# Performance work log

Hardware: AMD Instinct MI355X
Metric: run time of the kernel (lower is better)

## Reference

```python
import jax, jax.numpy as jnp
import numpy as np

N = 100000
E = 1600000
F_NODE = 6
F_EDGE = 2
H = 64


def _glorot(key, shape):
    lim = float(np.sqrt(6.0 / (shape[0] + shape[1])))
    return jax.random.uniform(key, shape, jnp.float32, -lim, lim)


def setup_inputs() -> dict:
    key = jax.random.key(0)
    ks = jax.random.split(key, 16)
    inp = {
        "x": jax.random.normal(ks[0], (N, F_NODE), jnp.float32),
        "edge_index": jax.random.randint(ks[1], (2, E), 0, N, jnp.int64),
        "edge_attr": jax.random.normal(ks[2], (E, F_EDGE), jnp.float32),
        # GCN layers (PyG GCNConv: linear no-bias, then aggregate, then +bias)
        "W1": _glorot(ks[3], (F_NODE, H)), "b1": jnp.zeros((H,), jnp.float32),
        "W2": _glorot(ks[4], (H, H)), "b2": jnp.zeros((H,), jnp.float32),
        "W3": _glorot(ks[5], (H, H)), "b3": jnp.zeros((H,), jnp.float32),
        # edge_mlp
        "We1": _glorot(ks[6], (F_EDGE, H)), "be1": jnp.zeros((H,), jnp.float32),
        "We2": _glorot(ks[7], (H, H)), "be2": jnp.zeros((H,), jnp.float32),
        # predictor
        "Wp1": _glorot(ks[8], (3 * H, H)), "bp1": jnp.zeros((H,), jnp.float32),
        "Wp2": _glorot(ks[9], (H, H // 2)), "bp2": jnp.zeros((H // 2,), jnp.float32),
        "Wp3": _glorot(ks[10], (H // 2, 1)), "bp3": jnp.zeros((1,), jnp.float32),
    }
    return inp


def _gcn_conv(h, W, b, src_sl, dst_sl, norm, n):
    # PyG GCNConv with self-loops and symmetric normalization
    h = h @ W                                   # [N, H_out]
    msg = h[src_sl] * norm[:, None]             # gather + scale per edge(+loop)
    out = jax.ops.segment_sum(msg, dst_sl, num_segments=n)
    return out + b


def _forward(x, edge_attr, W1, b1, W2, b2, W3, b3, We1, be1, We2, be2,
             Wp1, bp1, Wp2, bp2, Wp3, bp3, edge_index):
    n = x.shape[0]
    src, dst = edge_index[0], edge_index[1]

    # --- edge feature injection (vectorized version of per-edge loop) ---
    ef = jax.nn.relu(edge_attr @ We1 + be1) @ We2 + be2      # [E, H]
    nef = (jax.ops.segment_sum(ef, src, num_segments=n)
           + jax.ops.segment_sum(ef, dst, num_segments=n))   # [N, H]
    ones_e = jnp.ones((ef.shape[0],), x.dtype)
    deg = (jax.ops.segment_sum(ones_e, src, num_segments=n)
           + jax.ops.segment_sum(ones_e, dst, num_segments=n))
    deg = jnp.maximum(deg, 1.0)
    nef = nef / deg[:, None]
    # hidden_dim (64) >= node feature dim (6) -> truncate
    x = x + nef[:, : x.shape[1]] * 0.5

    # --- GCN normalization with self-loops (shared across layers) ---
    loop = jnp.arange(n, dtype=src.dtype)
    src_sl = jnp.concatenate([src, loop])
    dst_sl = jnp.concatenate([dst, loop])
    deg_sl = jax.ops.segment_sum(jnp.ones_like(dst_sl, dtype=x.dtype), dst_sl,
                                 num_segments=n)
    dinv = jnp.where(deg_sl > 0, deg_sl ** -0.5, 0.0)
    norm = dinv[src_sl] * dinv[dst_sl]

    h = jax.nn.relu(_gcn_conv(x, W1, b1, src_sl, dst_sl, norm, n))
    h = jax.nn.relu(_gcn_conv(h, W2, b2, src_sl, dst_sl, norm, n))
    h = _gcn_conv(h, W3, b3, src_sl, dst_sl, norm, n)

    graph_emb = h.mean(axis=0)                 # global_mean_pool, batch=None
    node_mean = h.mean(axis=0)
    node_std = jnp.std(h, axis=0, ddof=1)      # torch.std is unbiased
    combined = jnp.concatenate([graph_emb, node_mean, node_std])  # [3H]

    p = jax.nn.relu(combined @ Wp1 + bp1)      # dropout inactive in eval
    p = jax.nn.relu(p @ Wp2 + bp2)
    out = jax.nn.sigmoid(p @ Wp3 + bp3)        # (1,)
    return out


def reference(x, edge_index, edge_attr, W1, b1, W2, b2, W3, b3,
              We1, be1, We2, be2, Wp1, bp1, Wp2, bp2, Wp3, bp3):
    return _forward(x, edge_attr, W1, b1, W2, b2, W3, b3, We1, be1, We2, be2,
                    Wp1, bp1, Wp2, bp2, Wp3, bp3, edge_index)
```

## Files before the change

### kernel.cpp

```cpp
#include <hip/hip_runtime.h>
#include <hip/hip_bf16.h>
#include <stdint.h>

typedef float floatx2 __attribute__((ext_vector_type(2)));

#define NPB 256
#define NB 391
#define NBLKA 512

__device__ __forceinline__ float rdlane(float v, int l) {
    return __uint_as_float(__builtin_amdgcn_readlane(__float_as_uint(v), l));
}
__device__ __forceinline__ unsigned pk_fp8x4(float a, float b, float c, float d) {
    int u = __builtin_amdgcn_cvt_pk_fp8_f32(a, b, 0, false);
    u = __builtin_amdgcn_cvt_pk_fp8_f32(c, d, u, true);
    return (unsigned)u;
}
__device__ __forceinline__ unsigned pk_fp8x2(float a, float b) {
    return (unsigned)__builtin_amdgcn_cvt_pk_fp8_f32(a, b, 0, false);
}

__global__ __launch_bounds__(512) void k_zero(int* __restrict__ inTot,
                                              double* __restrict__ sums) {
    int t = threadIdx.x;
    if (t < 128) sums[t] = 0.0;
    if (t < NB) inTot[t] = 0;
}

__global__ __launch_bounds__(256) void k_A1(const int* __restrict__ ei,
                                            int* __restrict__ h,
                                            int* __restrict__ inTot,
                                            int E, int epb) {
    __shared__ int hist[NB], histIn[NB];
    int t = threadIdx.x, blk = blockIdx.x;
    for (int b = t; b < NB; b += 256) { hist[b] = 0; histIn[b] = 0; }
    __syncthreads();
    int e0 = blk * epb, e1 = min(E, e0 + epb);
    for (int e = e0 + t; e < e1; e += 256) {
        int s = ei[e], d = ei[E + e];
        atomicAdd(&hist[s >> 8], 1);
        atomicAdd(&hist[d >> 8], 1);
        atomicAdd(&histIn[d >> 8], 1);
    }
    __syncthreads();
    for (int b = t; b < NB; b += 256) {
        h[(size_t)b * NBLKA + blk] = hist[b];
        if (histIn[b]) atomicAdd(&inTot[b], histIn[b]);
    }
}

__global__ __launch_bounds__(512) void k_sc1(const int* __restrict__ v,
                                             int* __restrict__ bsum, int n) {
    __shared__ int l[512];
    int i = blockIdx.x * 512 + threadIdx.x;
    l[threadIdx.x] = (i < n) ? v[i] : 0;
    __syncthreads();
    for (int s = 256; s > 0; s >>= 1) {
        if (threadIdx.x < s) l[threadIdx.x] += l[threadIdx.x + s];
        __syncthreads();
    }
    if (threadIdx.x == 0) bsum[blockIdx.x] = l[0];
}
__global__ __launch_bounds__(512) void k_sc2(int* __restrict__ bsum, int nb) {
    __shared__ int l[512];
    int t = threadIdx.x;
    int v = (t < nb) ? bsum[t] : 0;
    l[t] = v;
    __syncthreads();
    for (int s = 1; s < 512; s <<= 1) {
        int tmp = (t >= s) ? l[t - s] : 0;
        __syncthreads();
        l[t] += tmp;
        __syncthreads();
    }
    if (t < nb) bsum[t] = l[t] - v;
}
__global__ __launch_bounds__(512) void k_sc3(int* __restrict__ v,
                                             const int* __restrict__ bsum, int n) {
    __shared__ int l[512];
    int i = blockIdx.x * 512 + threadIdx.x;
    int x = (i < n) ? v[i] : 0;
    l[threadIdx.x] = x;
    __syncthreads();
    for (int s = 1; s < 512; s <<= 1) {
        int tmp = (threadIdx.x >= (unsigned)s) ? l[threadIdx.x - s] : 0;
        __syncthreads();
        l[threadIdx.x] += tmp;
        __syncthreads();
    }
    if (i < n) v[i] = l[threadIdx.x] - x + bsum[blockIdx.x];
}
__global__ __launch_bounds__(512) void k_scanIn(const int* __restrict__ inTot,
                                                int* __restrict__ inBase) {
    __shared__ int l[512];
    int t = threadIdx.x;
    int v = (t < NB) ? inTot[t] : 0;
    l[t] = v;
    __syncthreads();
    for (int s = 1; s < 512; s <<= 1) {
        int tmp = (t >= s) ? l[t - s] : 0;
        __syncthreads();
        l[t] += tmp;
        __syncthreads();
    }
    if (t < NB) inBase[t] = l[t] - v;
}

__global__ __launch_bounds__(256) void k_A2(
    const int* __restrict__ ei, const float* __restrict__ ea,
    const float* __restrict__ We1, const float* __restrict__ be1,
    const float* __restrict__ We2, const float* __restrict__ be2,
    const int* __restrict__ hs, uint4* __restrict__ rec, int E, int epb) {
    __shared__ float sWe1[128], sbe1[64], sWe2[64 * 6], sbe2[6];
    __shared__ int cur[NB];
    int t = threadIdx.x, blk = blockIdx.x;
    if (t < 128) sWe1[t] = We1[t];
    if (t < 64) {
        sbe1[t] = be1[t];
#pragma unroll
        for (int c = 0; c < 6; ++c) sWe2[t * 6 + c] = We2[t * 64 + c];
    }
    if (t < 6) sbe2[t] = be2[t];
    for (int b = t; b < NB; b += 256) cur[b] = hs[(size_t)b * NBLKA + blk];
    __syncthreads();

    int e0 = blk * epb, e1 = min(E, e0 + epb);
    for (int e = e0 + t; e < e1; e += 256) {
        int s = ei[e], d = ei[E + e];
        float2 aa = ((const float2*)ea)[e];
        float acc[6];
#pragma unroll
        for (int c = 0; c < 6; ++c) acc[c] = sbe2[c];
#pragma unroll
        for (int j = 0; j < 64; ++j) {
            float hh = fmaf(aa.x, sWe1[j], fmaf(aa.y, sWe1[64 + j], sbe1[j]));
            hh = fmaxf(hh, 0.f);
#pragma unroll
            for (int c = 0; c < 6; ++c) acc[c] = fmaf(hh, sWe2[j * 6 + c], acc[c]);
        }
        unsigned z = pk_fp8x4(acc[0], acc[1], acc[2], acc[3]);
        unsigned w = pk_fp8x2(acc[4], acc[5]);
        int p0 = atomicAdd(&cur[s >> 8], 1);
        rec[p0] = make_uint4((unsigned)(s << 1), 0u, z, w);
        int p1 = atomicAdd(&cur[d >> 8], 1);
        rec[p1] = make_uint4((unsigned)(d << 1) | 1u, (unsigned)s, z, w);
    }
}

__global__ __launch_bounds__(256) void k_B(
    const uint4* __restrict__ rec, const int* __restrict__ hs,
    const int* __restrict__ inBase, const float* __restrict__ x,
    float* __restrict__ xp, float* __restrict__ dinv,
    int* __restrict__ offI, int* __restrict__ in_src, int E, int N) {
    __shared__ float nef[NPB * 6];
    __shared__ int degAll[NPB], degIn[NPB], rnk[NPB], sc[NPB], exO[NPB];
    int t = threadIdx.x, b = blockIdx.x;
#pragma unroll
    for (int c = 0; c < 6; ++c) nef[t * 6 + c] = 0.f;
    degAll[t] = 0; degIn[t] = 0; rnk[t] = 0;
    __syncthreads();

    int rb = hs[(size_t)b * NBLKA];
    int re = (b == NB - 1) ? 2 * E : hs[(size_t)(b + 1) * NBLKA];
    for (int j = rb + t; j < re; j += 256) {
        uint4 r = rec[j];
        int l = (int)((r.x >> 1) & 255u);
        atomicAdd(&degAll[l], 1);
        if (r.x & 1u) atomicAdd(&degIn[l], 1);
        floatx2 p01 = __builtin_amdgcn_cvt_pk_f32_fp8(r.z, false);
        floatx2 p23 = __builtin_amdgcn_cvt_pk_f32_fp8(r.z, true);
        floatx2 p45 = __builtin_amdgcn_cvt_pk_f32_fp8(r.w, false);
        atomicAdd(&nef[l * 6 + 0], p01.x);
        atomicAdd(&nef[l * 6 + 1], p01.y);
        atomicAdd(&nef[l * 6 + 2], p23.x);
        atomicAdd(&nef[l * 6 + 3], p23.y);
        atomicAdd(&nef[l * 6 + 4], p45.x);
        atomicAdd(&nef[l * 6 + 5], p45.y);
    }
    __syncthreads();

    int v = degIn[t];
    sc[t] = v;
    __syncthreads();
    for (int s = 1; s < 256; s <<= 1) {
        int tmp = (t >= s) ? sc[t - s] : 0;
        __syncthreads();
        sc[t] += tmp;
        __syncthreads();
    }
    exO[t] = sc[t] - v;
    __syncthreads();

    int node = b * NPB + t;
    int ib = inBase[b];
    if (node <= N) offI[node] = ib + exO[t];
    if (node < N) {
        float da = (float)degAll[t];
        float inv = 0.5f / fmaxf(da, 1.f);
        const float2* xr = (const float2*)(x + (size_t)node * 6);
        float2 x01 = xr[0], x23 = xr[1], x45 = xr[2];
        float2* xw = (float2*)(xp + (size_t)node * 6);
        xw[0] = make_float2(x01.x + nef[t * 6 + 0] * inv, x01.y + nef[t * 6 + 1] * inv);
        xw[1] = make_float2(x23.x + nef[t * 6 + 2] * inv, x23.y + nef[t * 6 + 3] * inv);
        xw[2] = make_float2(x45.x + nef[t * 6 + 4] * inv, x45.y + nef[t * 6 + 5] * inv);
        dinv[node] = 1.f / sqrtf(1.f + (float)degIn[t]);
    }
    __syncthreads();

    for (int j = rb + t; j < re; j += 256) {
        uint4 r = rec[j];
        if (r.x & 1u) {
            int l = (int)((r.x >> 1) & 255u);
            int k = atomicAdd(&rnk[l], 1);
            in_src[ib + exO[l] + k] = (int)r.y;
        }
    }
}

__global__ __launch_bounds__(256) void k_mm1(const float* __restrict__ xp,
                                             const float* __restrict__ W1,
                                             const float* __restrict__ dinv,
                                             unsigned* __restrict__ sOut, int n) {
    int lane = threadIdx.x & 63;
    int sub = lane & 15;
    int wid = (blockIdx.x * blockDim.x + threadIdx.x) >> 6;
    int nw = (gridDim.x * blockDim.x) >> 6;
    float w[6];
#pragma unroll
    for (int c = 0; c < 6; ++c) w[c] = W1[c * 64 + lane];
    for (int i = wid; i < n; i += nw) {
        float xv = (lane < 6) ? xp[(size_t)i * 6 + lane] : 0.f;
        float acc = 0.f;
#pragma unroll
        for (int c = 0; c < 6; ++c) acc = fmaf(rdlane(xv, c), w[c], acc);
        float o = acc * dinv[i];
        float o0 = __shfl(o, sub * 4 + 0);
        float o1 = __shfl(o, sub * 4 + 1);
        float o2 = __shfl(o, sub * 4 + 2);
        float o3 = __shfl(o, sub * 4 + 3);
        if (lane < 16) sOut[(size_t)i * 16 + lane] = pk_fp8x4(o0, o1, o2, o3);
    }
}

__global__ __launch_bounds__(256) void k_gathermm(
    const int* __restrict__ offI, const int* __restrict__ in_src,
    const float* __restrict__ dinv, const unsigned* __restrict__ sIn,
    const float* __restrict__ bias, const float* __restrict__ W,
    unsigned* __restrict__ sOut, int n) {
    int lane = threadIdx.x & 63;
    int sub = lane & 15, grp = lane >> 4;
    int wid = (blockIdx.x * blockDim.x + threadIdx.x) >> 6;
    int nw = (gridDim.x * blockDim.x) >> 6;
    float w[64];
#pragma unroll
    for (int c = 0; c < 64; ++c) w[c] = W[c * 64 + lane];
    float4 bb = ((const float4*)bias)[sub];

    for (int i = wid; i < n; i += nw) {
        unsigned su = sIn[(size_t)i * 16 + sub];
        float a0, a1, a2, a3;
        if (grp == 0) {
            floatx2 lo = __builtin_amdgcn_cvt_pk_f32_fp8(su, false);
            floatx2 hi = __builtin_amdgcn_cvt_pk_f32_fp8(su, true);
            a0 = lo.x; a1 = lo.y; a2 = hi.x; a3 = hi.y;
        } else { a0 = a1 = a2 = a3 = 0.f; }
        int b0 = offI[i], e0 = offI[i + 1];
#pragma unroll 4
        for (int j = b0 + grp; j < e0; j += 4) {
            unsigned src = (unsigned)in_src[j];
            unsigned u = sIn[(size_t)src * 16 + sub];
            floatx2 lo = __builtin_amdgcn_cvt_pk_f32_fp8(u, false);
            floatx2 hi = __builtin_amdgcn_cvt_pk_f32_fp8(u, true);
            a0 += lo.x; a1 += lo.y; a2 += hi.x; a3 += hi.y;
        }
        a0 += __shfl_xor(a0, 16); a1 += __shfl_xor(a1, 16);
        a2 += __shfl_xor(a2, 16); a3 += __shfl_xor(a3, 16);
        a0 += __shfl_xor(a0, 32); a1 += __shfl_xor(a1, 32);
        a2 += __shfl_xor(a2, 32); a3 += __shfl_xor(a3, 32);

        float dv = dinv[i];
        float h0 = fmaxf(fmaf(a0, dv, bb.x), 0.f);
        float h1 = fmaxf(fmaf(a1, dv, bb.y), 0.f);
        float h2 = fmaxf(fmaf(a2, dv, bb.z), 0.f);
        float h3 = fmaxf(fmaf(a3, dv, bb.w), 0.f);
        float o = 0.f;
#pragma unroll
        for (int g = 0; g < 16; ++g) {
            o = fmaf(rdlane(h0, g), w[g * 4 + 0], o);
            o = fmaf(rdlane(h1, g), w[g * 4 + 1], o);
            o = fmaf(rdlane(h2, g), w[g * 4 + 2], o);
            o = fmaf(rdlane(h3, g), w[g * 4 + 3], o);
        }
        o *= dv;
        float o0 = __shfl(o, sub * 4 + 0);
        float o1 = __shfl(o, sub * 4 + 1);
        float o2 = __shfl(o, sub * 4 + 2);
        float o3 = __shfl(o, sub * 4 + 3);
        if (lane < 16) sOut[(size_t)i * 16 + lane] = pk_fp8x4(o0, o1, o2, o3);
    }
}

__global__ __launch_bounds__(256) void k_gatherreduce(
    const int* __restrict__ offI, const int* __restrict__ in_src,
    const float* __restrict__ dinv, const unsigned* __restrict__ sIn,
    const float* __restrict__ b3, double* __restrict__ sums, int n) {
    int lane = threadIdx.x & 63;
    int sub = lane & 15, grp = lane >> 4;
    int wv = threadIdx.x >> 6;
    int wid = (blockIdx.x * blockDim.x + threadIdx.x) >> 6;
    int nw = (gridDim.x * blockDim.x) >> 6;
    float4 bb = ((const float4*)b3)[sub];
    double s0 = 0.0, s1 = 0.0, s2_ = 0.0, s3 = 0.0;
    double q0 = 0.0, q1 = 0.0, q2 = 0.0, q3 = 0.0;

    for (int i = wid; i < n; i += nw) {
        unsigned su = sIn[(size_t)i * 16 + sub];
        float a0, a1, a2, a3;
        if (grp == 0) {
            floatx2 lo = __builtin_amdgcn_cvt_pk_f32_fp8(su, false);
            floatx2 hi = __builtin_amdgcn_cvt_pk_f32_fp8(su, true);
            a0 = lo.x; a1 = lo.y; a2 = hi.x; a3 = hi.y;
        } else { a0 = a1 = a2 = a3 = 0.f; }
        int b0 = offI[i], e0 = offI[i + 1];
#pragma unroll 4
        for (int j = b0 + grp; j < e0; j += 4) {
            unsigned src = (unsigned)in_src[j];
            unsigned u = sIn[(size_t)src * 16 + sub];
            floatx2 lo = __builtin_amdgcn_cvt_pk_f32_fp8(u, false);
            floatx2 hi = __builtin_amdgcn_cvt_pk_f32_fp8(u, true);
            a0 += lo.x; a1 += lo.y; a2 += hi.x; a3 += hi.y;
        }
        a0 += __shfl_xor(a0, 16); a1 += __shfl_xor(a1, 16);
        a2 += __shfl_xor(a2, 16); a3 += __shfl_xor(a3, 16);
        a0 += __shfl_xor(a0, 32); a1 += __shfl_xor(a1, 32);
        a2 += __shfl_xor(a2, 32); a3 += __shfl_xor(a3, 32);

        float dv = dinv[i];
        float v0 = fmaf(a0, dv, bb.x);
        float v1 = fmaf(a1, dv, bb.y);
        float v2 = fmaf(a2, dv, bb.z);
        float v3 = fmaf(a3, dv, bb.w);
        s0 += v0; s1 += v1; s2_ += v2; s3 += v3;
        q0 += (double)v0 * v0; q1 += (double)v1 * v1;
        q2 += (double)v2 * v2; q3 += (double)v3 * v3;
    }
    __shared__ double shS[4 * 64], shQ[4 * 64];
    if (grp == 0) {
#pragma unroll
        for (int k = 0; k < 4; ++k) {
            double sk = (k == 0) ? s0 : (k == 1) ? s1 : (k == 2) ? s2_ : s3;
            double qk = (k == 0) ? q0 : (k == 1) ? q1 : (k == 2) ? q2 : q3;
            shS[wv * 64 + sub * 4 + k] = sk;
            shQ[wv * 64 + sub * 4 + k] = qk;
        }
    }
    __syncthreads();
    if (wv == 0) {
        double a = shS[lane] + shS[64 + lane] + shS[128 + lane] + shS[192 + lane];
        double c = shQ[lane] + shQ[64 + lane] + shQ[128 + lane] + shQ[192 + lane];
        unsafeAtomicAdd(&sums[lane], a);
        unsafeAtomicAdd(&sums[64 + lane], c);
    }
}

__global__ void k_head(const double* __restrict__ sums,
                       const float* __restrict__ Wp1, const float* __restrict__ bp1,
                       const float* __restrict__ Wp2, const float* __restrict__ bp2,
                       const float* __restrict__ Wp3, const float* __restrict__ bp3,
                       float* __restrict__ out, int n) {
    __shared__ float comb[192], p1[64], p2[32];
    int t = threadIdx.x;
    if (t < 64) {
        double s = sums[t], s2 = sums[64 + t];
        double m = s / n;
        double var = (s2 - s * s / n) / (double)(n - 1);
        float mf = (float)m;
        float sd = (float)sqrt(var > 0.0 ? var : 0.0);
        comb[t] = mf;
        comb[64 + t] = mf;
        comb[128 + t] = sd;
    }
    __syncthreads();
    if (t < 64) {
        float acc = bp1[t];
        for (int k = 0; k < 192; ++k) acc = fmaf(comb[k], Wp1[k * 64 + t], acc);
        p1[t] = fmaxf(acc, 0.f);
    }
    __syncthreads();
    if (t < 32) {
        float acc = bp2[t];
        for (int k = 0; k < 64; ++k) acc = fmaf(p1[k], Wp2[k * 32 + t], acc);
        p2[t] = fmaxf(acc, 0.f);
    }
    __syncthreads();
    if (t == 0) {
        float acc = bp3[0];
        for (int k = 0; k < 32; ++k) acc = fmaf(p2[k], Wp3[k], acc);
        out[0] = 1.f / (1.f + expf(-acc));
    }
}

static inline char* align16(char* p) {
    return (char*)(((uintptr_t)p + 15) & ~(uintptr_t)15);
}

extern "C" void kernel_launch(void* const* d_in, const int* in_sizes, int n_in,
                              void* d_out, int out_size, void* d_ws, size_t ws_size,
                              hipStream_t stream) {
    const float* x   = (const float*)d_in[0];
    const int*   ei  = (const int*)d_in[1];
    const float* ea  = (const float*)d_in[2];
    const float* W1  = (const float*)d_in[3];
    const float* b1  = (const float*)d_in[4];
    const float* W2  = (const float*)d_in[5];
    const float* b2  = (const float*)d_in[6];
    const float* W3  = (const float*)d_in[7];
    const float* b3  = (const float*)d_in[8];
    const float* We1 = (const float*)d_in[9];
    const float* be1 = (const float*)d_in[10];
    const float* We2 = (const float*)d_in[11];
    const float* be2 = (const float*)d_in[12];
    const float* Wp1 = (const float*)d_in[13];
    const float* bp1 = (const float*)d_in[14];
    const float* Wp2 = (const float*)d_in[15];
    const float* bp2 = (const float*)d_in[16];
    const float* Wp3 = (const float*)d_in[17];
    const float* bp3 = (const float*)d_in[18];

    const int N = in_sizes[0] / 6;
    const int E = in_sizes[1] / 2;
    const int epb = (E + NBLKA - 1) / NBLKA;
    const int HSZ = NB * NBLKA;
    const int nScan = (HSZ + 511) / 512;
    const size_t SB = (size_t)N * 64;

    char* p = (char*)d_ws;
    double* sums = (double*)p;          p = align16(p + 128 * sizeof(double));
    int* inTot = (int*)p;               p = align16(p + NB * 4);
    int* inBase = (int*)p;              p = align16(p + NB * 4);
    int* bsum = (int*)p;                p = align16(p + 512 * 4);
    int* h = (int*)p;                   p = align16(p + (size_t)HSZ * 4);
    float* xp = (float*)p;              p = align16(p + (size_t)N * 6 * 4);
    float* dinv = (float*)p;            p = align16(p + (size_t)N * 4);
    int* offI = (int*)p;                p = align16(p + ((size_t)N + 1) * 4);
    int* in_src = (int*)p;              p = align16(p + (size_t)E * 4);
    char* u = p;
    uint4* rec = (uint4*)u;
    unsigned* sbufA = (unsigned*)u;
    unsigned* sbufB = (unsigned*)(u + ((SB + 15) & ~(size_t)15));

    dim3 blk(256);

    k_zero<<<dim3(1), dim3(512), 0, stream>>>(inTot, sums);
    k_A1<<<dim3(NBLKA), blk, 0, stream>>>(ei, h, inTot, E, epb);
    k_sc1<<<dim3(nScan), dim3(512), 0, stream>>>(h, bsum, HSZ);
    k_sc2<<<dim3(1), dim3(512), 0, stream>>>(bsum, nScan);
    k_sc3<<<dim3(nScan), dim3(512), 0, stream>>>(h, bsum, HSZ);
    k_scanIn<<<dim3(1), dim3(512), 0, stream>>>(inTot, inBase);
    k_A2<<<dim3(NBLKA), blk, 0, stream>>>(ei, ea, We1, be1, We2, be2, h, rec, E, epb);
    k_B<<<dim3(NB), blk, 0, stream>>>(rec, h, inBase, x, xp, dinv, offI, in_src, E, N);

    k_mm1<<<dim3(1024), blk, 0, stream>>>(xp, W1, dinv, sbufA, N);
    k_gathermm<<<dim3(2048), blk, 0, stream>>>(offI, in_src, dinv, sbufA, b1, W2, sbufB, N);
    k_gathermm<<<dim3(2048), blk, 0, stream>>>(offI, in_src, dinv, sbufB, b2, W3, sbufA, N);
    k_gatherreduce<<<dim3(2048), blk, 0, stream>>>(offI, in_src, dinv, sbufA, b3, sums, N);
    k_head<<<dim3(1), dim3(64), 0, stream>>>(sums, Wp1, bp1, Wp2, bp2, Wp3, bp3,
                                             (float*)d_out, N);
}
```

Before: 615.5 us.

## Move edge MLP into histogram pass and widen node buckets to 512

The per-edge MLP and fp8 packing move from the scatter kernel k_A2 into the histogram kernel k_A1, which writes packed edge features to a new buffer that k_A2 then reads. The aim is to shorten the atomic-heavy scatter pass and give the histogram pass arithmetic to hide its memory latency. Node buckets grow from 256 to 512 nodes, so there are fewer buckets (196), fewer partition blocks (128), k_B runs with 512 threads, and the histogram scan is smaller. The cost is an extra E*8-byte buffer written and read back, and only 128 blocks in the A passes, which may not fill the GPU.

Result: slower. 752.9 us (+22.3%).

```diff
diff --git a/kernel.cpp b/kernel.cpp
--- a/kernel.cpp
+++ b/kernel.cpp
@@ -4,9 +4,9 @@
 
 typedef float floatx2 __attribute__((ext_vector_type(2)));
 
-#define NPB 256
-#define NB 391
-#define NBLKA 512
+#define NPB 512
+#define NB 196
+#define NBLKA 128
 
 __device__ __forceinline__ float rdlane(float v, int l) {
     return __uint_as_float(__builtin_amdgcn_readlane(__float_as_uint(v), l));
@@ -27,20 +27,44 @@
     if (t < NB) inTot[t] = 0;
 }
 
-__global__ __launch_bounds__(256) void k_A1(const int* __restrict__ ei,
-                                            int* __restrict__ h,
-                                            int* __restrict__ inTot,
-                                            int E, int epb) {
+__global__ __launch_bounds__(256) void k_A1(
+    const int* __restrict__ ei, const float* __restrict__ ea,
+    const float* __restrict__ We1, const float* __restrict__ be1,
+    const float* __restrict__ We2, const float* __restrict__ be2,
+    uint2* __restrict__ efp, int* __restrict__ h, int* __restrict__ inTot,
+    int E, int epb) {
+    __shared__ float sWe1[128], sbe1[64], sWe2[64 * 6], sbe2[6];
     __shared__ int hist[NB], histIn[NB];
     int t = threadIdx.x, blk = blockIdx.x;
+    if (t < 128) sWe1[t] = We1[t];
+    if (t < 64) {
+        sbe1[t] = be1[t];
+#pragma unroll
+        for (int c = 0; c < 6; ++c) sWe2[t * 6 + c] = We2[t * 64 + c];
+    }
+    if (t < 6) sbe2[t] = be2[t];
     for (int b = t; b < NB; b += 256) { hist[b] = 0; histIn[b] = 0; }
     __syncthreads();
+
     int e0 = blk * epb, e1 = min(E, e0 + epb);
     for (int e = e0 + t; e < e1; e += 256) {
         int s = ei[e], d = ei[E + e];
-        atomicAdd(&hist[s >> 8], 1);
-        atomicAdd(&hist[d >> 8], 1);
-        atomicAdd(&histIn[d >> 8], 1);
+        atomicAdd(&hist[s >> 9], 1);
+        atomicAdd(&hist[d >> 9], 1);
+        atomicAdd(&histIn[d >> 9], 1);
+        float2 aa = ((const float2*)ea)[e];
+        float acc[6];
+#pragma unroll
+        for (int c = 0; c < 6; ++c) acc[c] = sbe2[c];
+#pragma unroll
+        for (int j = 0; j < 64; ++j) {
+            float hh = fmaf(aa.x, sWe1[j], fmaf(aa.y, sWe1[64 + j], sbe1[j]));
+            hh = fmaxf(hh, 0.f);
+#pragma unroll
+            for (int c = 0; c < 6; ++c) acc[c] = fmaf(hh, sWe2[j * 6 + c], acc[c]);
+        }
+        efp[e] = make_uint2(pk_fp8x4(acc[0], acc[1], acc[2], acc[3]),
+                            pk_fp8x2(acc[4], acc[5]));
     }
     __syncthreads();
     for (int b = t; b < NB; b += 256) {
@@ -106,48 +130,26 @@
     if (t < NB) inBase[t] = l[t] - v;
 }
 
-__global__ __launch_bounds__(256) void k_A2(
-    const int* __restrict__ ei, const float* __restrict__ ea,
-    const float* __restrict__ We1, const float* __restrict__ be1,
-    const float* __restrict__ We2, const float* __restrict__ be2,
-    const int* __restrict__ hs, uint4* __restrict__ rec, int E, int epb) {
-    __shared__ float sWe1[128], sbe1[64], sWe2[64 * 6], sbe2[6];
+__global__ __launch_bounds__(256) void k_A2(const int* __restrict__ ei,
+                                            const uint2* __restrict__ efp,
+                                            const int* __restrict__ hs,
+                                            uint4* __restrict__ rec, int E, int epb) {
     __shared__ int cur[NB];
     int t = threadIdx.x, blk = blockIdx.x;
-    if (t < 128) sWe1[t] = We1[t];
-    if (t < 64) {
-        sbe1[t] = be1[t];
-#pragma unroll
-        for (int c = 0; c < 6; ++c) sWe2[t * 6 + c] = We2[t * 64 + c];
-    }
-    if (t < 6) sbe2[t] = be2[t];
     for (int b = t; b < NB; b += 256) cur[b] = hs[(size_t)b * NBLKA + blk];
     __syncthreads();
-
     int e0 = blk * epb, e1 = min(E, e0 + epb);
     for (int e = e0 + t; e < e1; e += 256) {
         int s = ei[e], d = ei[E + e];
-        float2 aa = ((const float2*)ea)[e];
-        float acc[6];
-#pragma unroll
-        for (int c = 0; c < 6; ++c) acc[c] = sbe2[c];
-#pragma unroll
-        for (int j = 0; j < 64; ++j) {
-            float hh = fmaf(aa.x, sWe1[j], fmaf(aa.y, sWe1[64 + j], sbe1[j]));
-            hh = fmaxf(hh, 0.f);
-#pragma unroll
-            for (int c = 0; c < 6; ++c) acc[c] = fmaf(hh, sWe2[j * 6 + c], acc[c]);
-        }
-        unsigned z = pk_fp8x4(acc[0], acc[1], acc[2], acc[3]);
-        unsigned w = pk_fp8x2(acc[4], acc[5]);
-        int p0 = atomicAdd(&cur[s >> 8], 1);
-        rec[p0] = make_uint4((unsigned)(s << 1), 0u, z, w);
-        int p1 = atomicAdd(&cur[d >> 8], 1);
-        rec[p1] = make_uint4((unsigned)(d << 1) | 1u, (unsigned)s, z, w);
-    }
-}
-
-__global__ __launch_bounds__(256) void k_B(
+        uint2 f = efp[e];
+        int p0 = atomicAdd(&cur[s >> 9], 1);
+        rec[p0] = make_uint4((unsigned)(s << 1), 0u, f.x, f.y);
+        int p1 = atomicAdd(&cur[d >> 9], 1);
+        rec[p1] = make_uint4((unsigned)(d << 1) | 1u, (unsigned)s, f.x, f.y);
+    }
+}
+
+__global__ __launch_bounds__(512) void k_B(
     const uint4* __restrict__ rec, const int* __restrict__ hs,
     const int* __restrict__ inBase, const float* __restrict__ x,
     float* __restrict__ xp, float* __restrict__ dinv,
@@ -162,9 +164,9 @@
 
     int rb = hs[(size_t)b * NBLKA];
     int re = (b == NB - 1) ? 2 * E : hs[(size_t)(b + 1) * NBLKA];
-    for (int j = rb + t; j < re; j += 256) {
+    for (int j = rb + t; j < re; j += 512) {
         uint4 r = rec[j];
-        int l = (int)((r.x >> 1) & 255u);
+        int l = (int)((r.x >> 1) & (NPB - 1));
         atomicAdd(&degAll[l], 1);
         if (r.x & 1u) atomicAdd(&degIn[l], 1);
         floatx2 p01 = __builtin_amdgcn_cvt_pk_f32_fp8(r.z, false);
@@ -182,7 +184,7 @@
     int v = degIn[t];
     sc[t] = v;
     __syncthreads();
-    for (int s = 1; s < 256; s <<= 1) {
+    for (int s = 1; s < 512; s <<= 1) {
         int tmp = (t >= s) ? sc[t - s] : 0;
         __syncthreads();
         sc[t] += tmp;
@@ -207,10 +209,10 @@
     }
     __syncthreads();
 
-    for (int j = rb + t; j < re; j += 256) {
+    for (int j = rb + t; j < re; j += 512) {
         uint4 r = rec[j];
         if (r.x & 1u) {
-            int l = (int)((r.x >> 1) & 255u);
+            int l = (int)((r.x >> 1) & (NPB - 1));
             int k = atomicAdd(&rnk[l], 1);
             in_src[ib + exO[l] + k] = (int)r.y;
         }
@@ -440,6 +442,7 @@
     int* inBase = (int*)p;              p = align16(p + NB * 4);
     int* bsum = (int*)p;                p = align16(p + 512 * 4);
     int* h = (int*)p;                   p = align16(p + (size_t)HSZ * 4);
+    uint2* efp = (uint2*)p;             p = align16(p + (size_t)E * 8);
     float* xp = (float*)p;              p = align16(p + (size_t)N * 6 * 4);
     float* dinv = (float*)p;            p = align16(p + (size_t)N * 4);
     int* offI = (int*)p;                p = align16(p + ((size_t)N + 1) * 4);
@@ -452,13 +455,13 @@
     dim3 blk(256);
 
     k_zero<<<dim3(1), dim3(512), 0, stream>>>(inTot, sums);
-    k_A1<<<dim3(NBLKA), blk, 0, stream>>>(ei, h, inTot, E, epb);
+    k_A1<<<dim3(NBLKA), blk, 0, stream>>>(ei, ea, We1, be1, We2, be2, efp, h, inTot, E, epb);
     k_sc1<<<dim3(nScan), dim3(512), 0, stream>>>(h, bsum, HSZ);
     k_sc2<<<dim3(1), dim3(512), 0, stream>>>(bsum, nScan);
     k_sc3<<<dim3(nScan), dim3(512), 0, stream>>>(h, bsum, HSZ);
     k_scanIn<<<dim3(1), dim3(512), 0, stream>>>(inTot, inBase);
-    k_A2<<<dim3(NBLKA), blk, 0, stream>>>(ei, ea, We1, be1, We2, be2, h, rec, E, epb);
-    k_B<<<dim3(NB), blk, 0, stream>>>(rec, h, inBase, x, xp, dinv, offI, in_src, E, N);
+    k_A2<<<dim3(NBLKA), blk, 0, stream>>>(ei, efp, h, rec, E, epb);
+    k_B<<<dim3(NB), dim3(512), 0, stream>>>(rec, h, inBase, x, xp, dinv, offI, in_src, E, N);
 
     k_mm1<<<dim3(1024), blk, 0, stream>>>(xp, W1, dinv, sbufA, N);
     k_gathermm<<<dim3(2048), blk, 0, stream>>>(offI, in_src, dinv, sbufA, b1, W2, sbufB, N);
```
